# Kernel optimization log

Measured on AMD Instinct MI355X. Metric: run time of the kernel, lower is better.

The kernel has to match this reference:

```python
import jax, jax.numpy as jnp
import numpy as np

B, S, HID = 4, 8192, 1024
H = 32          # num heads == num kv heads
D = HID // H    # head_dim (== H, required by original broadcast)


def setup_inputs() -> dict:
    key = jax.random.key(0)
    ks = jax.random.split(key, 8)
    sc = 1.0 / np.sqrt(HID)
    return {
        "hidden_states": jax.random.normal(ks[0], (B, S, HID), jnp.float32),
        "wq": jax.random.normal(ks[1], (HID, HID), jnp.float32) * sc,
        "wk": jax.random.normal(ks[2], (HID, HID), jnp.float32) * sc,
        "wv": jax.random.normal(ks[3], (HID, HID), jnp.float32) * sc,
        "wo": jax.random.normal(ks[4], (HID, HID), jnp.float32) * sc,
        "mu_q": jnp.zeros((H,), jnp.float32),
        "sigma_q": jnp.ones((H,), jnp.float32),
        "mu_kv": jnp.zeros((H,), jnp.float32),
        "sigma_kv": jnp.ones((H,), jnp.float32),
        "eps_q": jax.random.normal(ks[5], (H,), jnp.float32),
        "eps_kv": jax.random.normal(ks[6], (H,), jnp.float32),
    }


def _kl(mu, sigma):
    return -0.5 * jnp.mean(1.0 + sigma - mu * mu - jnp.exp(sigma))


def reference(hidden_states, wq, wk, wv, wo, mu_q, sigma_q, mu_kv, sigma_kv, eps_q, eps_kv):
    # projections (torch Linear: y = x @ W.T)
    q = (hidden_states @ wq.T).reshape(B, S, H, D)
    k = (hidden_states @ wk.T).reshape(B, S, H, D)
    v = (hidden_states @ wv.T).reshape(B, S, H, D)
    # VIB masks; NOTE: original code broadcasts mask (shape [H]) over the
    # LAST axis (head_dim) of q/k/v -- faithful since D == H here.
    mask_q = jax.nn.sigmoid(mu_q + eps_q * sigma_q)    # [D]
    mask_kv = jax.nn.sigmoid(mu_kv + eps_kv * sigma_kv)  # [D]
    q = q * mask_q
    k = k * mask_kv
    v = v * mask_kv
    # per-token head-vs-head attention: scores [B,S,H,H]
    scores = jnp.einsum("bshd,bstd->bsht", q, k) / np.sqrt(D)
    w = jax.nn.softmax(scores, axis=-1)
    attn = jnp.einsum("bsht,bstd->bshd", w, v).reshape(B, S, HID)
    out = attn @ wo.T
    kl = _kl(mu_q, sigma_q) + _kl(mu_kv, sigma_kv)
    return out, kl
```

## Files before the change

kernel.cpp:

```cpp
#include <hip/hip_runtime.h>

typedef unsigned int uint32;
typedef unsigned short u16;
typedef __attribute__((ext_vector_type(4))) float f32x4;
typedef __attribute__((ext_vector_type(8))) short bf16x8;

#define HID 1024
#define NTOK 32768

__device__ __forceinline__ u16 f2bf(float f) {
    uint32 u = __builtin_bit_cast(uint32, f);
    u += 0x7FFFu + ((u >> 16) & 1u);
    return (u16)(u >> 16);
}
__device__ __forceinline__ float bf2f(u16 h) {
    uint32 u = ((uint32)h) << 16;
    return __builtin_bit_cast(float, u);
}

__device__ __forceinline__ void async16(const void* g, void* l) {
    __builtin_amdgcn_global_load_lds(
        (const __attribute__((address_space(1))) uint32*)g,
        (__attribute__((address_space(3))) uint32*)l, 16, 0, 0);
}

__global__ __launch_bounds__(256) void split_kernel(const float* __restrict__ x,
                                                    u16* __restrict__ hi,
                                                    u16* __restrict__ lo,
                                                    int n) {
    int i = (blockIdx.x * 256 + threadIdx.x) * 4;
    if (i >= n) return;
    float4 v = *reinterpret_cast<const float4*>(x + i);
    u16 h0 = f2bf(v.x), h1 = f2bf(v.y), h2 = f2bf(v.z), h3 = f2bf(v.w);
    u16 l0 = f2bf(v.x - bf2f(h0)), l1 = f2bf(v.y - bf2f(h1));
    u16 l2 = f2bf(v.z - bf2f(h2)), l3 = f2bf(v.w - bf2f(h3));
    *reinterpret_cast<uint2*>(hi + i) =
        make_uint2((uint32)h0 | ((uint32)h1 << 16), (uint32)h2 | ((uint32)h3 << 16));
    *reinterpret_cast<uint2*>(lo + i) =
        make_uint2((uint32)l0 | ((uint32)l1 << 16), (uint32)l2 | ((uint32)l3 << 16));
}

__device__ __forceinline__ void gemm_body(const u16* __restrict__ Ahi,
                                          const u16* __restrict__ Alo,
                                          const u16* __restrict__ Bhi,
                                          const u16* __restrict__ Blo,
                                          float* __restrict__ C) {
    __shared__ u16 sAh[128 * 32], sAl[128 * 32], sBh[128 * 32], sBl[128 * 32];
    const int tid = threadIdx.x;
    const int wave = tid >> 6, lane = tid & 63;
    const int m0 = blockIdx.x * 128, n0 = blockIdx.y * 128;
    const int wm = (wave >> 1) * 64, wn = (wave & 1) * 64;
    const int srow = lane >> 2;
    const int scol = ((lane & 3) ^ ((lane >> 3) & 3)) * 8;
    const int fr = lane & 15;
    const int ks = (((lane >> 4) ^ ((lane >> 1) & 3)) & 3) * 8;

    f32x4 acc[4][4];
#pragma unroll
    for (int a = 0; a < 4; a++)
#pragma unroll
        for (int b = 0; b < 4; b++) acc[a][b] = f32x4{0.f, 0.f, 0.f, 0.f};

    for (int k0 = 0; k0 < HID; k0 += 32) {
#pragma unroll
        for (int i = 0; i < 2; i++) {
            const int seg = wave * 2 + i;
            const int r = seg * 16 + srow;
            const size_t ga = (size_t)(m0 + r) * HID + k0 + scol;
            const size_t gb = (size_t)(n0 + r) * HID + k0 + scol;
            async16(Ahi + ga, &sAh[seg * 512]);
            async16(Alo + ga, &sAl[seg * 512]);
            async16(Bhi + gb, &sBh[seg * 512]);
            async16(Blo + gb, &sBl[seg * 512]);
        }
        __syncthreads();

        bf16x8 fah[4], fal[4], fbh[4], fbl[4];
#pragma unroll
        for (int a = 0; a < 4; a++) {
            const int row = wm + a * 16 + fr;
            fah[a] = *reinterpret_cast<const bf16x8*>(&sAh[row * 32 + ks]);
            fal[a] = *reinterpret_cast<const bf16x8*>(&sAl[row * 32 + ks]);
        }
#pragma unroll
        for (int b = 0; b < 4; b++) {
            const int row = wn + b * 16 + fr;
            fbh[b] = *reinterpret_cast<const bf16x8*>(&sBh[row * 32 + ks]);
            fbl[b] = *reinterpret_cast<const bf16x8*>(&sBl[row * 32 + ks]);
        }
#pragma unroll
        for (int a = 0; a < 4; a++)
#pragma unroll
            for (int b = 0; b < 4; b++)
                acc[a][b] = __builtin_amdgcn_mfma_f32_16x16x32_bf16(fah[a], fbh[b], acc[a][b], 0, 0, 0);
#pragma unroll
        for (int a = 0; a < 4; a++)
#pragma unroll
            for (int b = 0; b < 4; b++)
                acc[a][b] = __builtin_amdgcn_mfma_f32_16x16x32_bf16(fah[a], fbl[b], acc[a][b], 0, 0, 0);
#pragma unroll
        for (int a = 0; a < 4; a++)
#pragma unroll
            for (int b = 0; b < 4; b++)
                acc[a][b] = __builtin_amdgcn_mfma_f32_16x16x32_bf16(fal[a], fbh[b], acc[a][b], 0, 0, 0);
        __syncthreads();
    }

    const int col = lane & 15, r0 = (lane >> 4) * 4;
#pragma unroll
    for (int a = 0; a < 4; a++)
#pragma unroll
        for (int b = 0; b < 4; b++)
#pragma unroll
            for (int j = 0; j < 4; j++)
                C[(size_t)(m0 + wm + a * 16 + r0 + j) * HID + (n0 + wn + b * 16 + col)] =
                    acc[a][b][j];
}

__global__ __launch_bounds__(256) void gemm_qkv(
    const u16* __restrict__ xhi, const u16* __restrict__ xlo,
    const u16* __restrict__ w0h, const u16* __restrict__ w0l,
    const u16* __restrict__ w1h, const u16* __restrict__ w1l,
    const u16* __restrict__ w2h, const u16* __restrict__ w2l,
    float* __restrict__ q, float* __restrict__ k, float* __restrict__ v) {
    const u16 *bh, *bl;
    float* c;
    if (blockIdx.z == 0)      { bh = w0h; bl = w0l; c = q; }
    else if (blockIdx.z == 1) { bh = w1h; bl = w1l; c = k; }
    else                      { bh = w2h; bl = w2l; c = v; }
    gemm_body(xhi, xlo, bh, bl, c);
}

__global__ __launch_bounds__(256) void gemm_one(
    const u16* __restrict__ ahi, const u16* __restrict__ alo,
    const u16* __restrict__ bh, const u16* __restrict__ bl,
    float* __restrict__ c) {
    gemm_body(ahi, alo, bh, bl, c);
}

__global__ __launch_bounds__(256) void attn_kernel(
    const float* __restrict__ Q, const float* __restrict__ K, const float* __restrict__ V,
    const float* __restrict__ mu_q, const float* __restrict__ sigma_q,
    const float* __restrict__ mu_kv, const float* __restrict__ sigma_kv,
    const float* __restrict__ eps_q, const float* __restrict__ eps_kv,
    u16* __restrict__ Ohi, u16* __restrict__ Olo) {
    __shared__ float sm[4][3][32 * 33];
    __shared__ float mq[32], mkv[32];
    const int tid = threadIdx.x, wave = tid >> 6, lane = tid & 63;

    if (tid < 32) {
        mq[tid] = 1.f / (1.f + __expf(-(mu_q[tid] + eps_q[tid] * sigma_q[tid])));
    } else if (tid < 64) {
        const int d = tid - 32;
        mkv[d] = 1.f / (1.f + __expf(-(mu_kv[d] + eps_kv[d] * sigma_kv[d])));
    }
    __syncthreads();

    const size_t T = (size_t)blockIdx.x * 4 + wave;
    const float* src0 = Q + T * HID;
    const float* src1 = K + T * HID;
    const float* src2 = V + T * HID;
#pragma unroll
    for (int m = 0; m < 3; m++) {
        const float* s = (m == 0) ? src0 : (m == 1) ? src1 : src2;
        const float* msk = (m == 0) ? mq : mkv;
#pragma unroll
        for (int i = 0; i < 4; i++) {
            const int e = (i * 64 + lane) * 4;
            float4 v4 = *reinterpret_cast<const float4*>(s + e);
            const int r = e >> 5, c = e & 31;
            float* dst = &sm[wave][m][r * 33 + c];
            dst[0] = v4.x * msk[c];
            dst[1] = v4.y * msk[c + 1];
            dst[2] = v4.z * msk[c + 2];
            dst[3] = v4.w * msk[c + 3];
        }
    }
    __syncthreads();

    const int h = lane >> 1, half = lane & 1;
    float qreg[32];
    const float* qr = &sm[wave][0][h * 33];
#pragma unroll
    for (int d = 0; d < 32; d++) qreg[d] = qr[d];

    float sc[16];
    const float* kr = &sm[wave][1][0];
#pragma unroll
    for (int t1 = 0; t1 < 16; t1++) {
        const int t = half * 16 + t1;
        float a = 0.f;
#pragma unroll
        for (int d = 0; d < 32; d++) a += qreg[d] * kr[t * 33 + d];
        sc[t1] = a * 0.17677669529663687f;
    }
    float mx = sc[0];
#pragma unroll
    for (int t1 = 1; t1 < 16; t1++) mx = fmaxf(mx, sc[t1]);
    mx = fmaxf(mx, __shfl_xor(mx, 1));
    float sum = 0.f;
#pragma unroll
    for (int t1 = 0; t1 < 16; t1++) {
        sc[t1] = __expf(sc[t1] - mx);
        sum += sc[t1];
    }
    sum += __shfl_xor(sum, 1);
    const float inv = 1.f / sum;
    float* wrow = &sm[wave][0][h * 33];
#pragma unroll
    for (int t1 = 0; t1 < 16; t1++) wrow[half * 16 + t1] = sc[t1] * inv;
    __syncthreads();

    float acc[16];
#pragma unroll
    for (int j = 0; j < 16; j++) acc[j] = 0.f;
    const float* vr = &sm[wave][2][0];
#pragma unroll 4
    for (int t = 0; t < 32; t++) {
        const float wv = wrow[t];
#pragma unroll
        for (int j = 0; j < 16; j++) acc[j] += wv * vr[t * 33 + half * 16 + j];
    }

    u16 hs[16], ls[16];
#pragma unroll
    for (int j = 0; j < 16; j++) {
        hs[j] = f2bf(acc[j]);
        ls[j] = f2bf(acc[j] - bf2f(hs[j]));
    }
    const size_t base = T * HID + h * 32 + half * 16;
    uint32 ph[8], pl[8];
#pragma unroll
    for (int j = 0; j < 8; j++) {
        ph[j] = (uint32)hs[2 * j] | ((uint32)hs[2 * j + 1] << 16);
        pl[j] = (uint32)ls[2 * j] | ((uint32)ls[2 * j + 1] << 16);
    }
    *reinterpret_cast<uint4*>(Ohi + base)     = make_uint4(ph[0], ph[1], ph[2], ph[3]);
    *reinterpret_cast<uint4*>(Ohi + base + 8) = make_uint4(ph[4], ph[5], ph[6], ph[7]);
    *reinterpret_cast<uint4*>(Olo + base)     = make_uint4(pl[0], pl[1], pl[2], pl[3]);
    *reinterpret_cast<uint4*>(Olo + base + 8) = make_uint4(pl[4], pl[5], pl[6], pl[7]);
}

__global__ void kl_kernel(const float* __restrict__ mu_q, const float* __restrict__ sigma_q,
                          const float* __restrict__ mu_kv, const float* __restrict__ sigma_kv,
                          float* __restrict__ out) {
    const int l = threadIdx.x;
    float t;
    if (l < 32) {
        t = 1.f + sigma_q[l] - mu_q[l] * mu_q[l] - expf(sigma_q[l]);
    } else {
        const int d = l - 32;
        t = 1.f + sigma_kv[d] - mu_kv[d] * mu_kv[d] - expf(sigma_kv[d]);
    }
    t *= -0.5f / 32.f;
#pragma unroll
    for (int o = 32; o > 0; o >>= 1) t += __shfl_down(t, o);
    if (l == 0) out[0] = t;
}

extern "C" void kernel_launch(void* const* d_in, const int* in_sizes, int n_in,
                              void* d_out, int out_size, void* d_ws, size_t ws_size,
                              hipStream_t stream) {
    const float* hidden   = (const float*)d_in[0];
    const float* wq       = (const float*)d_in[1];
    const float* wk       = (const float*)d_in[2];
    const float* wv       = (const float*)d_in[3];
    const float* wo       = (const float*)d_in[4];
    const float* mu_q     = (const float*)d_in[5];
    const float* sigma_q  = (const float*)d_in[6];
    const float* mu_kv    = (const float*)d_in[7];
    const float* sigma_kv = (const float*)d_in[8];
    const float* eps_q    = (const float*)d_in[9];
    const float* eps_kv   = (const float*)d_in[10];
    float* out = (float*)d_out;

    const size_t WN = (size_t)HID * HID;
    const size_t WBYTES = 8 * WN * 2;
    int CH = NTOK;
    while (CH > 128 && WBYTES + (size_t)CH * 16384 > ws_size) CH >>= 1;

    char* ws = (char*)d_ws;
    u16* wsp = (u16*)ws;
    u16 *wqh = wsp + 0 * WN, *wql = wsp + 1 * WN;
    u16 *wkh = wsp + 2 * WN, *wkl = wsp + 3 * WN;
    u16 *wvh = wsp + 4 * WN, *wvl = wsp + 5 * WN;
    u16 *woh = wsp + 6 * WN, *wol = wsp + 7 * WN;
    char* dyn = ws + WBYTES;
    u16*   xh = (u16*)dyn;
    u16*   xl = xh + (size_t)CH * HID;
    float* q  = (float*)(xl + (size_t)CH * HID);
    float* k  = q + (size_t)CH * HID;
    float* v  = k + (size_t)CH * HID;

    split_kernel<<<1024, 256, 0, stream>>>(wq, wqh, wql, HID * HID);
    split_kernel<<<1024, 256, 0, stream>>>(wk, wkh, wkl, HID * HID);
    split_kernel<<<1024, 256, 0, stream>>>(wv, wvh, wvl, HID * HID);
    split_kernel<<<1024, 256, 0, stream>>>(wo, woh, wol, HID * HID);

    const int nchunks = NTOK / CH;
    for (int c = 0; c < nchunks; ++c) {
        const size_t off = (size_t)c * CH * HID;
        split_kernel<<<CH, 256, 0, stream>>>(hidden + off, xh, xl, CH * HID);
        dim3 gqkv(CH / 128, HID / 128, 3);
        gemm_qkv<<<gqkv, 256, 0, stream>>>(xh, xl, wqh, wql, wkh, wkl, wvh, wvl, q, k, v);
        attn_kernel<<<CH / 4, 256, 0, stream>>>(q, k, v, mu_q, sigma_q, mu_kv, sigma_kv,
                                                eps_q, eps_kv, xh, xl);
        dim3 gout(CH / 128, HID / 128, 1);
        gemm_one<<<gout, 256, 0, stream>>>(xh, xl, woh, wol, out + off);
    }

    kl_kernel<<<1, 64, 0, stream>>>(mu_q, sigma_q, mu_kv, sigma_kv, out + (out_size - 1));
}
```

Baseline: 1.324 ms.

## Double-buffer LDS tiles in split-bf16 GEMM and raise MFMA wave priority

Splits the shared-memory A/B hi/lo tiles into two buffers so the async global-to-LDS loads for the next K-slice are issued before computing on the current slice, leaving one barrier per iteration. It also wraps the MFMA block in s_setprio(1)/s_setprio(0) so waves doing matrix math get scheduling priority. The goal is to hide global load latency behind MFMA work. LDS use per block doubles to 64 KB, which may reduce occupancy. A single barrier still orders reads of the current buffer against the next prefetch into it, but it relies on the async loads completing by the barrier.

```diff
diff --git a/kernel.cpp b/kernel.cpp
--- a/kernel.cpp
+++ b/kernel.cpp
@@ -45,7 +45,8 @@
                                           const u16* __restrict__ Bhi,
                                           const u16* __restrict__ Blo,
                                           float* __restrict__ C) {
-    __shared__ u16 sAh[128 * 32], sAl[128 * 32], sBh[128 * 32], sBl[128 * 32];
+    __shared__ u16 sAh[2][128 * 32], sAl[2][128 * 32];
+    __shared__ u16 sBh[2][128 * 32], sBl[2][128 * 32];
     const int tid = threadIdx.x;
     const int wave = tid >> 6, lane = tid & 63;
     const int m0 = blockIdx.x * 128, n0 = blockIdx.y * 128;
@@ -55,39 +56,64 @@
     const int fr = lane & 15;
     const int ks = (((lane >> 4) ^ ((lane >> 1) & 3)) & 3) * 8;
 
+    const int seg0 = wave * 2, seg1 = wave * 2 + 1;
+    const int r0g = seg0 * 16 + srow, r1g = seg1 * 16 + srow;
+
     f32x4 acc[4][4];
 #pragma unroll
     for (int a = 0; a < 4; a++)
 #pragma unroll
         for (int b = 0; b < 4; b++) acc[a][b] = f32x4{0.f, 0.f, 0.f, 0.f};
 
+    {
+        const size_t ga0 = (size_t)(m0 + r0g) * HID + scol;
+        const size_t ga1 = (size_t)(m0 + r1g) * HID + scol;
+        const size_t gb0 = (size_t)(n0 + r0g) * HID + scol;
+        const size_t gb1 = (size_t)(n0 + r1g) * HID + scol;
+        async16(Ahi + ga0, &sAh[0][seg0 * 512]);
+        async16(Ahi + ga1, &sAh[0][seg1 * 512]);
+        async16(Alo + ga0, &sAl[0][seg0 * 512]);
+        async16(Alo + ga1, &sAl[0][seg1 * 512]);
+        async16(Bhi + gb0, &sBh[0][seg0 * 512]);
+        async16(Bhi + gb1, &sBh[0][seg1 * 512]);
+        async16(Blo + gb0, &sBl[0][seg0 * 512]);
+        async16(Blo + gb1, &sBl[0][seg1 * 512]);
+    }
+    __syncthreads();
+
+    int cur = 0;
     for (int k0 = 0; k0 < HID; k0 += 32) {
-#pragma unroll
-        for (int i = 0; i < 2; i++) {
-            const int seg = wave * 2 + i;
-            const int r = seg * 16 + srow;
-            const size_t ga = (size_t)(m0 + r) * HID + k0 + scol;
-            const size_t gb = (size_t)(n0 + r) * HID + k0 + scol;
-            async16(Ahi + ga, &sAh[seg * 512]);
-            async16(Alo + ga, &sAl[seg * 512]);
-            async16(Bhi + gb, &sBh[seg * 512]);
-            async16(Blo + gb, &sBl[seg * 512]);
+        if (k0 + 32 < HID) {
+            const int nxt = cur ^ 1;
+            const size_t ga0 = (size_t)(m0 + r0g) * HID + (k0 + 32) + scol;
+            const size_t ga1 = (size_t)(m0 + r1g) * HID + (k0 + 32) + scol;
+            const size_t gb0 = (size_t)(n0 + r0g) * HID + (k0 + 32) + scol;
+            const size_t gb1 = (size_t)(n0 + r1g) * HID + (k0 + 32) + scol;
+            async16(Ahi + ga0, &sAh[nxt][seg0 * 512]);
+            async16(Ahi + ga1, &sAh[nxt][seg1 * 512]);
+            async16(Alo + ga0, &sAl[nxt][seg0 * 512]);
+            async16(Alo + ga1, &sAl[nxt][seg1 * 512]);
+            async16(Bhi + gb0, &sBh[nxt][seg0 * 512]);
+            async16(Bhi + gb1, &sBh[nxt][seg1 * 512]);
+            async16(Blo + gb0, &sBl[nxt][seg0 * 512]);
+            async16(Blo + gb1, &sBl[nxt][seg1 * 512]);
         }
-        __syncthreads();
 
         bf16x8 fah[4], fal[4], fbh[4], fbl[4];
 #pragma unroll
         for (int a = 0; a < 4; a++) {
             const int row = wm + a * 16 + fr;
-            fah[a] = *reinterpret_cast<const bf16x8*>(&sAh[row * 32 + ks]);
-            fal[a] = *reinterpret_cast<const bf16x8*>(&sAl[row * 32 + ks]);
+            fah[a] = *reinterpret_cast<const bf16x8*>(&sAh[cur][row * 32 + ks]);
+            fal[a] = *reinterpret_cast<const bf16x8*>(&sAl[cur][row * 32 + ks]);
         }
 #pragma unroll
         for (int b = 0; b < 4; b++) {
             const int row = wn + b * 16 + fr;
-            fbh[b] = *reinterpret_cast<const bf16x8*>(&sBh[row * 32 + ks]);
-            fbl[b] = *reinterpret_cast<const bf16x8*>(&sBl[row * 32 + ks]);
+            fbh[b] = *reinterpret_cast<const bf16x8*>(&sBh[cur][row * 32 + ks]);
+            fbl[b] = *reinterpret_cast<const bf16x8*>(&sBl[cur][row * 32 + ks]);
         }
+
+        __builtin_amdgcn_s_setprio(1);
 #pragma unroll
         for (int a = 0; a < 4; a++)
 #pragma unroll
@@ -103,17 +129,20 @@
 #pragma unroll
             for (int b = 0; b < 4; b++)
                 acc[a][b] = __builtin_amdgcn_mfma_f32_16x16x32_bf16(fal[a], fbh[b], acc[a][b], 0, 0, 0);
+        __builtin_amdgcn_s_setprio(0);
+
         __syncthreads();
-    }
-
-    const int col = lane & 15, r0 = (lane >> 4) * 4;
+        cur ^= 1;
+    }
+
+    const int col = lane & 15, rr = (lane >> 4) * 4;
 #pragma unroll
     for (int a = 0; a < 4; a++)
 #pragma unroll
         for (int b = 0; b < 4; b++)
 #pragma unroll
             for (int j = 0; j < 4; j++)
-                C[(size_t)(m0 + wm + a * 16 + r0 + j) * HID + (n0 + wn + b * 16 + col)] =
+                C[(size_t)(m0 + wm + a * 16 + rr + j) * HID + (n0 + wn + b * 16 + col)] =
                     acc[a][b][j];
 }
 
```

Measured after the change: 1.218 ms. -8.0%, faster.

## Restructure split-bf16 GEMM into 256x256 double-buffered tiles with phased prefetch

Applied to the files above, without the earlier changes.

Reworks the shared GEMM body to compute 256x256 output tiles with 512 threads (8 waves, 128x64 per wave). Shared memory is now double-buffered, and the loads for the next K-slice are issued during the MFMA phases of the current one. Each wave group loads a single matrix, and the kernel uses s_setprio around the MFMA bursts. The goal is to hide global-to-LDS latency and get more reuse per tile. In exchange it uses more registers (128 accumulator floats per lane), 128KB of LDS per block, and fewer blocks for small chunks.

```diff
diff --git a/kernel.cpp b/kernel.cpp
--- a/kernel.cpp
+++ b/kernel.cpp
@@ -7,6 +7,7 @@
 
 #define HID 1024
 #define NTOK 32768
+#define MFMA16 __builtin_amdgcn_mfma_f32_16x16x32_bf16
 
 __device__ __forceinline__ u16 f2bf(float f) {
     uint32 u = __builtin_bit_cast(uint32, f);
@@ -45,79 +46,110 @@
                                           const u16* __restrict__ Bhi,
                                           const u16* __restrict__ Blo,
                                           float* __restrict__ C) {
-    __shared__ u16 sAh[128 * 32], sAl[128 * 32], sBh[128 * 32], sBl[128 * 32];
+    __shared__ u16 smem[2][4 * 8192];
     const int tid = threadIdx.x;
-    const int wave = tid >> 6, lane = tid & 63;
-    const int m0 = blockIdx.x * 128, n0 = blockIdx.y * 128;
-    const int wm = (wave >> 1) * 64, wn = (wave & 1) * 64;
+    const int wid = tid >> 6, lane = tid & 63;
+    const int m0 = blockIdx.x * 256, n0 = blockIdx.y * 256;
+    const int wm = (wid >> 2) * 128, wn = (wid & 3) * 64;
     const int srow = lane >> 2;
     const int scol = ((lane & 3) ^ ((lane >> 3) & 3)) * 8;
     const int fr = lane & 15;
     const int ks = (((lane >> 4) ^ ((lane >> 1) & 3)) & 3) * 8;
 
-    f32x4 acc[4][4];
-#pragma unroll
-    for (int a = 0; a < 4; a++)
-#pragma unroll
-        for (int b = 0; b < 4; b++) acc[a][b] = f32x4{0.f, 0.f, 0.f, 0.f};
+    const int mat = wid >> 1;
+    const int sbase = (wid & 1) * 8;
+    const u16* gsrc = (mat == 0) ? Ahi : (mat == 1) ? Alo : (mat == 2) ? Bhi : Blo;
+    const int rbase = (mat < 2) ? m0 : n0;
+    const int lregion = mat * 8192;
+
+    f32x4 acc[8][4];
+#pragma unroll
+    for (int i = 0; i < 8; i++)
+#pragma unroll
+        for (int j = 0; j < 4; j++) acc[i][j] = f32x4{0.f, 0.f, 0.f, 0.f};
+
+#pragma unroll
+    for (int j = 0; j < 8; j++)
+        async16(gsrc + (size_t)(rbase + (sbase + j) * 16 + srow) * HID + scol,
+                &smem[0][lregion + (sbase + j) * 512]);
+    asm volatile("s_waitcnt vmcnt(0)" ::: "memory");
+    __builtin_amdgcn_s_barrier();
+    asm volatile("" ::: "memory");
 
     for (int k0 = 0; k0 < HID; k0 += 32) {
-#pragma unroll
-        for (int i = 0; i < 2; i++) {
-            const int seg = wave * 2 + i;
-            const int r = seg * 16 + srow;
-            const size_t ga = (size_t)(m0 + r) * HID + k0 + scol;
-            const size_t gb = (size_t)(n0 + r) * HID + k0 + scol;
-            async16(Ahi + ga, &sAh[seg * 512]);
-            async16(Alo + ga, &sAl[seg * 512]);
-            async16(Bhi + gb, &sBh[seg * 512]);
-            async16(Blo + gb, &sBl[seg * 512]);
+        const int buf = (k0 >> 5) & 1;
+        const int nbuf = buf ^ 1;
+        const bool notlast = (k0 + 32) < HID;
+        const u16* sb = smem[buf];
+        bf16x8 fbh[4], fbl[4];
+#pragma unroll
+        for (int ph = 0; ph < 4; ph++) {
+            if (ph == 0) {
+#pragma unroll
+                for (int jn = 0; jn < 4; jn++) {
+                    const int row = wn + jn * 16 + fr;
+                    fbh[jn] = *reinterpret_cast<const bf16x8*>(&sb[16384 + row * 32 + ks]);
+                    fbl[jn] = *reinterpret_cast<const bf16x8*>(&sb[24576 + row * 32 + ks]);
+                }
+            }
+            bf16x8 fah[2], fal[2];
+#pragma unroll
+            for (int ii = 0; ii < 2; ii++) {
+                const int row = wm + (ph * 2 + ii) * 16 + fr;
+                fah[ii] = *reinterpret_cast<const bf16x8*>(&sb[row * 32 + ks]);
+                fal[ii] = *reinterpret_cast<const bf16x8*>(&sb[8192 + row * 32 + ks]);
+            }
+            if (notlast && ph < 2) {
+#pragma unroll
+                for (int jj = 0; jj < 4; jj++) {
+                    const int j = ph * 4 + jj;
+                    async16(gsrc + (size_t)(rbase + (sbase + j) * 16 + srow) * HID +
+                                (k0 + 32) + scol,
+                            &smem[nbuf][lregion + (sbase + j) * 512]);
+                }
+            }
+            asm volatile("" ::: "memory");
+            __builtin_amdgcn_s_barrier();
+            asm volatile("" ::: "memory");
+
+            __builtin_amdgcn_s_setprio(1);
+#pragma unroll
+            for (int jn = 0; jn < 4; jn++)
+#pragma unroll
+                for (int ii = 0; ii < 2; ii++)
+                    acc[ph * 2 + ii][jn] = MFMA16(fah[ii], fbh[jn], acc[ph * 2 + ii][jn], 0, 0, 0);
+#pragma unroll
+            for (int jn = 0; jn < 4; jn++)
+#pragma unroll
+                for (int ii = 0; ii < 2; ii++)
+                    acc[ph * 2 + ii][jn] = MFMA16(fah[ii], fbl[jn], acc[ph * 2 + ii][jn], 0, 0, 0);
+#pragma unroll
+            for (int jn = 0; jn < 4; jn++)
+#pragma unroll
+                for (int ii = 0; ii < 2; ii++)
+                    acc[ph * 2 + ii][jn] = MFMA16(fal[ii], fbh[jn], acc[ph * 2 + ii][jn], 0, 0, 0);
+            __builtin_amdgcn_s_setprio(0);
+
+            asm volatile("" ::: "memory");
+            if (ph == 3 && notlast)
+                asm volatile("s_waitcnt vmcnt(0)" ::: "memory");
+            __builtin_amdgcn_s_barrier();
+            asm volatile("" ::: "memory");
         }
-        __syncthreads();
-
-        bf16x8 fah[4], fal[4], fbh[4], fbl[4];
-#pragma unroll
-        for (int a = 0; a < 4; a++) {
-            const int row = wm + a * 16 + fr;
-            fah[a] = *reinterpret_cast<const bf16x8*>(&sAh[row * 32 + ks]);
-            fal[a] = *reinterpret_cast<const bf16x8*>(&sAl[row * 32 + ks]);
-        }
-#pragma unroll
-        for (int b = 0; b < 4; b++) {
-            const int row = wn + b * 16 + fr;
-            fbh[b] = *reinterpret_cast<const bf16x8*>(&sBh[row * 32 + ks]);
-            fbl[b] = *reinterpret_cast<const bf16x8*>(&sBl[row * 32 + ks]);
-        }
-#pragma unroll
-        for (int a = 0; a < 4; a++)
-#pragma unroll
-            for (int b = 0; b < 4; b++)
-                acc[a][b] = __builtin_amdgcn_mfma_f32_16x16x32_bf16(fah[a], fbh[b], acc[a][b], 0, 0, 0);
-#pragma unroll
-        for (int a = 0; a < 4; a++)
-#pragma unroll
-            for (int b = 0; b < 4; b++)
-                acc[a][b] = __builtin_amdgcn_mfma_f32_16x16x32_bf16(fah[a], fbl[b], acc[a][b], 0, 0, 0);
-#pragma unroll
-        for (int a = 0; a < 4; a++)
-#pragma unroll
-            for (int b = 0; b < 4; b++)
-                acc[a][b] = __builtin_amdgcn_mfma_f32_16x16x32_bf16(fal[a], fbh[b], acc[a][b], 0, 0, 0);
-        __syncthreads();
-    }
-
-    const int col = lane & 15, r0 = (lane >> 4) * 4;
-#pragma unroll
-    for (int a = 0; a < 4; a++)
-#pragma unroll
-        for (int b = 0; b < 4; b++)
+    }
+
+    const int col = lane & 15, rr = (lane >> 4) * 4;
+#pragma unroll
+    for (int i = 0; i < 8; i++)
+#pragma unroll
+        for (int jn = 0; jn < 4; jn++)
 #pragma unroll
             for (int j = 0; j < 4; j++)
-                C[(size_t)(m0 + wm + a * 16 + r0 + j) * HID + (n0 + wn + b * 16 + col)] =
-                    acc[a][b][j];
-}
-
-__global__ __launch_bounds__(256) void gemm_qkv(
+                C[(size_t)(m0 + wm + i * 16 + rr + j) * HID + (n0 + wn + jn * 16 + col)] =
+                    acc[i][jn][j];
+}
+
+__global__ __launch_bounds__(512, 2) void gemm_qkv(
     const u16* __restrict__ xhi, const u16* __restrict__ xlo,
     const u16* __restrict__ w0h, const u16* __restrict__ w0l,
     const u16* __restrict__ w1h, const u16* __restrict__ w1l,
@@ -131,7 +163,7 @@
     gemm_body(xhi, xlo, bh, bl, c);
 }
 
-__global__ __launch_bounds__(256) void gemm_one(
+__global__ __launch_bounds__(512, 2) void gemm_one(
     const u16* __restrict__ ahi, const u16* __restrict__ alo,
     const u16* __restrict__ bh, const u16* __restrict__ bl,
     float* __restrict__ c) {
@@ -277,7 +309,7 @@
     const size_t WN = (size_t)HID * HID;
     const size_t WBYTES = 8 * WN * 2;
     int CH = NTOK;
-    while (CH > 128 && WBYTES + (size_t)CH * 16384 > ws_size) CH >>= 1;
+    while (CH > 256 && WBYTES + (size_t)CH * 16384 > ws_size) CH >>= 1;
 
     char* ws = (char*)d_ws;
     u16* wsp = (u16*)ws;
@@ -301,12 +333,12 @@
     for (int c = 0; c < nchunks; ++c) {
         const size_t off = (size_t)c * CH * HID;
         split_kernel<<<CH, 256, 0, stream>>>(hidden + off, xh, xl, CH * HID);
-        dim3 gqkv(CH / 128, HID / 128, 3);
-        gemm_qkv<<<gqkv, 256, 0, stream>>>(xh, xl, wqh, wql, wkh, wkl, wvh, wvl, q, k, v);
+        dim3 gqkv(CH / 256, HID / 256, 3);
+        gemm_qkv<<<gqkv, 512, 0, stream>>>(xh, xl, wqh, wql, wkh, wkl, wvh, wvl, q, k, v);
         attn_kernel<<<CH / 4, 256, 0, stream>>>(q, k, v, mu_q, sigma_q, mu_kv, sigma_kv,
                                                 eps_q, eps_kv, xh, xl);
-        dim3 gout(CH / 128, HID / 128, 1);
-        gemm_one<<<gout, 256, 0, stream>>>(xh, xl, woh, wol, out + off);
+        dim3 gout(CH / 256, HID / 256, 1);
+        gemm_one<<<gout, 512, 0, stream>>>(xh, xl, woh, wol, out + off);
     }
 
     kl_kernel<<<1, 64, 0, stream>>>(mu_q, sigma_q, mu_kv, sigma_kv, out + (out_size - 1));
```

Result: faster. 1.064 ms (-19.6%).
